# Optimization experiments

Measured on AMD Instinct MI355X. Metric: run time of the kernel, lower is better.

Reference implementation:

```python
import jax, jax.numpy as jnp
import numpy as np

TOP_K = 2
UP = 4  # upfeat(disp_4, spg, 4, 4)


def reference(cost, spg):
    """cost: [b,1,D,h,w] raw cost volume; spg: [b,9,4h,4w] superpixel logits.
    Returns disp_1: [b,4h,4w] (eval-mode output of CoExDispProcessor regression)."""
    b, _, D, h, w = cost.shape
    # spx_pred = softmax over the 9 neighbor channels
    prob = jax.nn.softmax(spg, axis=1)  # [b,9,4h,4w]

    # --- topkpool (k=2): sort desc along disparity, take top-k values+indices ---
    c = jnp.moveaxis(cost, 2, -1)  # [b,1,h,w,D]
    vals, ind = jax.lax.top_k(c, TOP_K)  # [b,1,h,w,k], sorted descending
    corr = jax.nn.softmax(vals, axis=-1)
    disp4 = jnp.sum(corr * ind.astype(cost.dtype), axis=-1)  # [b,1,h,w]

    pad = jnp.pad(disp4, ((0, 0), (0, 0), (1, 1), (1, 1)))
    # F.unfold ordering: kernel row-major, channel index = ki*3 + kj
    patches = jnp.stack(
        [pad[:, 0, i:i + h, j:j + w] for i in range(3) for j in range(3)],
        axis=1)  # [b,9,h,w]
    up = jnp.repeat(jnp.repeat(patches, UP, axis=2), UP, axis=3)  # [b,9,4h,4w]
    disp1 = jnp.sum(up * prob, axis=1) * 4.0  # [b,4h,4w], scaled to full-res disparity
    return disp1


def setup_inputs() -> dict:
    key = jax.random.key(0)
    k1, k2 = jax.random.split(key)
    b, D, h, w = 8, 48, 128, 240
    cost = jax.random.normal(k1, (b, 1, D, h, w), dtype=jnp.float32)
    spg = jax.random.normal(k2, (b, 9, 4 * h, 4 * w), dtype=jnp.float32)
    return {"cost": cost, "spg": spg}
```

## Files before the change

### kernel.cpp

```cpp
#include <hip/hip_runtime.h>
#include <math.h>

#define BB 8
#define DD 48
#define HH 128
#define WW 240
#define HW (HH * WW)
#define FH (4 * HH)
#define FW (4 * WW)
#define FHW (FH * FW)

typedef float vf2 __attribute__((ext_vector_type(2)));
typedef float vf4 __attribute__((ext_vector_type(4)));

__global__ __launch_bounds__(256) void disp4_kernel(const float* __restrict__ cost,
                                                    float* __restrict__ disp4) {
    int t = blockIdx.x * blockDim.x + threadIdx.x;
    const int WQ = WW / 2;
    if (t >= BB * HH * WQ) return;
    int wq = t % WQ;
    int r  = t / WQ;
    int hy = r % HH;
    int b  = r / HH;

    const float* base = cost + (size_t)b * DD * HW + (size_t)hy * WW + wq * 2;

    float m1[2], m2[2], i1[2], i2[2];
#pragma unroll
    for (int k = 0; k < 2; ++k) { m1[k] = -INFINITY; m2[k] = -INFINITY; i1[k] = 0.f; i2[k] = 0.f; }

#pragma unroll
    for (int dd = 0; dd < DD; dd += 8) {
        vf2 v[8];
#pragma unroll
        for (int u = 0; u < 8; ++u)
            v[u] = __builtin_nontemporal_load(
                reinterpret_cast<const vf2*>(base + (size_t)(dd + u) * HW));
#pragma unroll
        for (int u = 0; u < 8; ++u) {
            float fd = (float)(dd + u);
            float vv[2] = {v[u].x, v[u].y};
#pragma unroll
            for (int k = 0; k < 2; ++k) {
                bool g1 = vv[k] > m1[k];
                bool g2 = vv[k] > m2[k];
                m2[k] = g1 ? m1[k] : (g2 ? vv[k] : m2[k]);
                i2[k] = g1 ? i1[k] : (g2 ? fd    : i2[k]);
                m1[k] = g1 ? vv[k] : m1[k];
                i1[k] = g1 ? fd    : i1[k];
            }
        }
    }

    vf2 o;
#pragma unroll
    for (int k = 0; k < 2; ++k) {
        float e = __expf(m2[k] - m1[k]);
        float s = e / (1.f + e);
        o[k] = i1[k] + (i2[k] - i1[k]) * s;
    }
    *reinterpret_cast<vf2*>(disp4 + (size_t)b * HW + (size_t)hy * WW + wq * 2) = o;
}

__global__ __launch_bounds__(256) void upfeat_kernel(const float* __restrict__ spg,
                                                     const float* __restrict__ disp4,
                                                     float* __restrict__ out) {
    int t = blockIdx.x * blockDim.x + threadIdx.x;
    const int XQ = FW / 4;
    if (t >= BB * FH * XQ) return;
    int xq = t % XQ;
    int r  = t / XQ;
    int y  = r % FH;
    int b  = r / FH;
    int hy = y >> 2;

    float p[9];
#pragma unroll
    for (int i = 0; i < 3; ++i) {
#pragma unroll
        for (int j = 0; j < 3; ++j) {
            int cy = hy + i - 1;
            int cx = xq + j - 1;
            bool ok = (cy >= 0) & (cy < HH) & (cx >= 0) & (cx < WW);
            p[i * 3 + j] = ok ? disp4[(size_t)b * HW + (size_t)cy * WW + cx] : 0.f;
        }
    }

    const float* sp = spg + ((size_t)b * 9 * FH + (size_t)y) * FW + xq * 4;
    float s[9][4];
#pragma unroll
    for (int c = 0; c < 9; ++c) {
        vf4 v = __builtin_nontemporal_load(
            reinterpret_cast<const vf4*>(sp + (size_t)c * FHW));
        s[c][0] = v.x; s[c][1] = v.y; s[c][2] = v.z; s[c][3] = v.w;
    }

    vf4 ov;
#pragma unroll
    for (int k = 0; k < 4; ++k) {
        float m = s[0][k];
#pragma unroll
        for (int c = 1; c < 9; ++c) m = fmaxf(m, s[c][k]);
        float num = 0.f, den = 0.f;
#pragma unroll
        for (int c = 0; c < 9; ++c) {
            float e = __expf(s[c][k] - m);
            num = fmaf(e, p[c], num);
            den += e;
        }
        ov[k] = 4.f * __fdividef(num, den);
    }

    __builtin_nontemporal_store(ov, reinterpret_cast<vf4*>(
        out + ((size_t)b * FH + (size_t)y) * FW + xq * 4));
}

extern "C" void kernel_launch(void* const* d_in, const int* in_sizes, int n_in,
                              void* d_out, int out_size, void* d_ws, size_t ws_size,
                              hipStream_t stream) {
    const float* cost = (const float*)d_in[0];
    const float* spg  = (const float*)d_in[1];
    float* outp  = (float*)d_out;
    float* disp4 = (float*)d_ws;

    {
        int total = BB * HH * (WW / 2);
        int blocks = (total + 255) / 256;
        disp4_kernel<<<blocks, 256, 0, stream>>>(cost, disp4);
    }
    {
        int total = BB * FH * (FW / 4);
        int blocks = (total + 255) / 256;
        upfeat_kernel<<<blocks, 256, 0, stream>>>(spg, disp4, outp);
    }
}
```

Measured before the change: 218.4 us.

## Fuse top-k disparity regression and superpixel upsampling into one tiled kernel

Merges the two kernels into one that computes the low-res disparity for a tile plus halo into shared memory, then performs the 9-neighbour softmax-weighted upsampling from LDS. This removes the intermediate global buffer and a kernel launch. In exchange it recomputes halo pixels, uses scalar instead of vector cost loads, and launches only 512 blocks, which may reduce occupancy and memory-level parallelism.

Result: slower. 249.3 us (+14.1%).

```diff
diff --git a/kernel.cpp b/kernel.cpp
--- a/kernel.cpp
+++ b/kernel.cpp
@@ -10,109 +10,121 @@
 #define FW (4 * WW)
 #define FHW (FH * FW)
 
-typedef float vf2 __attribute__((ext_vector_type(2)));
+#define TW 60
+#define TH 8
+#define HALO_W (TW + 2)
+#define HALO_H (TH + 2)
+#define NPX (HALO_W * HALO_H)
+#define NQ  (TW * 4 * TH)
+
 typedef float vf4 __attribute__((ext_vector_type(4)));
 
-__global__ __launch_bounds__(256) void disp4_kernel(const float* __restrict__ cost,
-                                                    float* __restrict__ disp4) {
-    int t = blockIdx.x * blockDim.x + threadIdx.x;
-    const int WQ = WW / 2;
-    if (t >= BB * HH * WQ) return;
-    int wq = t % WQ;
-    int r  = t / WQ;
-    int hy = r % HH;
-    int b  = r / HH;
+__global__ __launch_bounds__(256) void fused_disp_kernel(const float* __restrict__ cost,
+                                                         const float* __restrict__ spg,
+                                                         float* __restrict__ out) {
+    __shared__ float ld[HALO_H][HALO_W];
 
-    const float* base = cost + (size_t)b * DD * HW + (size_t)hy * WW + wq * 2;
+    int tid = threadIdx.x;
+    int blk = blockIdx.x;
+    int bx = blk & 3;
+    int by = (blk >> 2) & 15;
+    int b  = blk >> 6;
+    int cw0 = bx * TW;
+    int ch0 = by * TH;
 
-    float m1[2], m2[2], i1[2], i2[2];
+    const float* cbase = cost + (size_t)b * DD * HW;
+    float m1[3], m2[3], i1[3], i2[3];
+    const float* addr[3];
+    bool inb[3], valid[3];
+    int hr_[3], hc_[3];
 #pragma unroll
-    for (int k = 0; k < 2; ++k) { m1[k] = -INFINITY; m2[k] = -INFINITY; i1[k] = 0.f; i2[k] = 0.f; }
-
+    for (int s = 0; s < 3; ++s) {
+        int idx = tid + s * 256;
+        valid[s] = idx < NPX;
+        int hr = valid[s] ? (idx / HALO_W) : 0;
+        int hc = valid[s] ? (idx - hr * HALO_W) : 0;
+        hr_[s] = hr; hc_[s] = hc;
+        int cy = ch0 + hr - 1;
+        int cx = cw0 + hc - 1;
+        inb[s] = valid[s] & (cy >= 0) & (cy < HH) & (cx >= 0) & (cx < WW);
+        addr[s] = inb[s] ? (cbase + (size_t)cy * WW + cx) : cbase;
+        m1[s] = -INFINITY; m2[s] = -INFINITY; i1[s] = 0.f; i2[s] = 0.f;
+    }
 #pragma unroll
-    for (int dd = 0; dd < DD; dd += 8) {
-        vf2 v[8];
+    for (int dd = 0; dd < DD; dd += 4) {
+        float v[4][3];
 #pragma unroll
-        for (int u = 0; u < 8; ++u)
-            v[u] = __builtin_nontemporal_load(
-                reinterpret_cast<const vf2*>(base + (size_t)(dd + u) * HW));
+        for (int u = 0; u < 4; ++u)
 #pragma unroll
-        for (int u = 0; u < 8; ++u) {
+            for (int s = 0; s < 3; ++s)
+                v[u][s] = addr[s][(size_t)(dd + u) * HW];
+#pragma unroll
+        for (int u = 0; u < 4; ++u) {
             float fd = (float)(dd + u);
-            float vv[2] = {v[u].x, v[u].y};
 #pragma unroll
-            for (int k = 0; k < 2; ++k) {
-                bool g1 = vv[k] > m1[k];
-                bool g2 = vv[k] > m2[k];
-                m2[k] = g1 ? m1[k] : (g2 ? vv[k] : m2[k]);
-                i2[k] = g1 ? i1[k] : (g2 ? fd    : i2[k]);
-                m1[k] = g1 ? vv[k] : m1[k];
-                i1[k] = g1 ? fd    : i1[k];
+            for (int s = 0; s < 3; ++s) {
+                float vv = v[u][s];
+                bool g1 = vv > m1[s];
+                bool g2 = vv > m2[s];
+                m2[s] = g1 ? m1[s] : (g2 ? vv : m2[s]);
+                i2[s] = g1 ? i1[s] : (g2 ? fd : i2[s]);
+                m1[s] = g1 ? vv : m1[s];
+                i1[s] = g1 ? fd : i1[s];
             }
         }
     }
-
-    vf2 o;
 #pragma unroll
-    for (int k = 0; k < 2; ++k) {
-        float e = __expf(m2[k] - m1[k]);
-        float s = e / (1.f + e);
-        o[k] = i1[k] + (i2[k] - i1[k]) * s;
-    }
-    *reinterpret_cast<vf2*>(disp4 + (size_t)b * HW + (size_t)hy * WW + wq * 2) = o;
-}
-
-__global__ __launch_bounds__(256) void upfeat_kernel(const float* __restrict__ spg,
-                                                     const float* __restrict__ disp4,
-                                                     float* __restrict__ out) {
-    int t = blockIdx.x * blockDim.x + threadIdx.x;
-    const int XQ = FW / 4;
-    if (t >= BB * FH * XQ) return;
-    int xq = t % XQ;
-    int r  = t / XQ;
-    int y  = r % FH;
-    int b  = r / FH;
-    int hy = y >> 2;
-
-    float p[9];
-#pragma unroll
-    for (int i = 0; i < 3; ++i) {
-#pragma unroll
-        for (int j = 0; j < 3; ++j) {
-            int cy = hy + i - 1;
-            int cx = xq + j - 1;
-            bool ok = (cy >= 0) & (cy < HH) & (cx >= 0) & (cx < WW);
-            p[i * 3 + j] = ok ? disp4[(size_t)b * HW + (size_t)cy * WW + cx] : 0.f;
+    for (int s = 0; s < 3; ++s) {
+        if (valid[s]) {
+            float e = __expf(m2[s] - m1[s]);
+            float sg = e / (1.f + e);
+            float dv = i1[s] + (i2[s] - i1[s]) * sg;
+            ld[hr_[s]][hc_[s]] = inb[s] ? dv : 0.f;
         }
     }
+    __syncthreads();
 
-    const float* sp = spg + ((size_t)b * 9 * FH + (size_t)y) * FW + xq * 4;
-    float s[9][4];
+    for (int q = tid; q < NQ; q += 256) {
+        int qx = q % TW;
+        int qy = q / TW;
+        int y  = 4 * ch0 + qy;
+        int hr = (qy >> 2);
+
+        float p[9];
 #pragma unroll
-    for (int c = 0; c < 9; ++c) {
-        vf4 v = __builtin_nontemporal_load(
-            reinterpret_cast<const vf4*>(sp + (size_t)c * FHW));
-        s[c][0] = v.x; s[c][1] = v.y; s[c][2] = v.z; s[c][3] = v.w;
-    }
+        for (int i = 0; i < 3; ++i)
+#pragma unroll
+            for (int j = 0; j < 3; ++j)
+                p[i * 3 + j] = ld[hr + i][qx + j];
 
-    vf4 ov;
-#pragma unroll
-    for (int k = 0; k < 4; ++k) {
-        float m = s[0][k];
-#pragma unroll
-        for (int c = 1; c < 9; ++c) m = fmaxf(m, s[c][k]);
-        float num = 0.f, den = 0.f;
+        const float* sp = spg + ((size_t)b * 9 * FH + y) * FW + (size_t)(cw0 + qx) * 4;
+        float s[9][4];
 #pragma unroll
         for (int c = 0; c < 9; ++c) {
-            float e = __expf(s[c][k] - m);
-            num = fmaf(e, p[c], num);
-            den += e;
+            vf4 v = __builtin_nontemporal_load(
+                reinterpret_cast<const vf4*>(sp + (size_t)c * FHW));
+            s[c][0] = v.x; s[c][1] = v.y; s[c][2] = v.z; s[c][3] = v.w;
         }
-        ov[k] = 4.f * __fdividef(num, den);
+
+        vf4 ov;
+#pragma unroll
+        for (int k = 0; k < 4; ++k) {
+            float m = s[0][k];
+#pragma unroll
+            for (int c = 1; c < 9; ++c) m = fmaxf(m, s[c][k]);
+            float num = 0.f, den = 0.f;
+#pragma unroll
+            for (int c = 0; c < 9; ++c) {
+                float e = __expf(s[c][k] - m);
+                num = fmaf(e, p[c], num);
+                den += e;
+            }
+            ov[k] = 4.f * __fdividef(num, den);
+        }
+
+        __builtin_nontemporal_store(ov, reinterpret_cast<vf4*>(
+            out + ((size_t)b * FH + y) * FW + (size_t)(cw0 + qx) * 4));
     }
-
-    __builtin_nontemporal_store(ov, reinterpret_cast<vf4*>(
-        out + ((size_t)b * FH + (size_t)y) * FW + xq * 4));
 }
 
 extern "C" void kernel_launch(void* const* d_in, const int* in_sizes, int n_in,
@@ -120,17 +132,8 @@
                               hipStream_t stream) {
     const float* cost = (const float*)d_in[0];
     const float* spg  = (const float*)d_in[1];
-    float* outp  = (float*)d_out;
-    float* disp4 = (float*)d_ws;
+    float* outp = (float*)d_out;
 
-    {
-        int total = BB * HH * (WW / 2);
-        int blocks = (total + 255) / 256;
-        disp4_kernel<<<blocks, 256, 0, stream>>>(cost, disp4);
-    }
-    {
-        int total = BB * FH * (FW / 4);
-        int blocks = (total + 255) / 256;
-        upfeat_kernel<<<blocks, 256, 0, stream>>>(spg, disp4, outp);
-    }
+    int blocks = 4 * 16 * BB;
+    fused_disp_kernel<<<blocks, 256, 0, stream>>>(cost, spg, outp);
 }
```
